# Performance work log

Hardware: AMD Instinct MI355X
Metric: run time of the kernel (lower is better)

The kernel has to match this reference:

```python
import math
import jax, jax.numpy as jnp
import numpy as np

CT = {"SDD": 1000.0, "SCD": 500.0, "det_interval": 1.0, "num_det": 736}


def ramp_filter_np(ct, scale):
    # Standard equiangular fan-beam ramp filter (utility.ramp_filter):
    #   h[0] = 1/(8*db^2); h[n odd] = -1/(2*(pi*sin(n*db))^2); h[n even!=0] = 0
    db = ct["det_interval"] / ct["SDD"] * scale  # angular detector pitch at this scale
    n_det = int(ct["num_det"] // scale)
    n = np.arange(-(n_det - 1), n_det)  # length K = 2*n_det - 1
    h = np.zeros(n.shape, dtype=np.float32)
    h[n == 0] = 1.0 / (8.0 * db ** 2)
    odd = (n % 2) != 0
    h[odd] = -0.5 / (np.pi * np.sin(n[odd] * db)) ** 2
    return h


def setup_inputs() -> dict:
    key = jax.random.key(0)
    scale = 1
    batch, ch, view, det = 16, 1, 1152, CT["num_det"] // scale
    sinogram = jax.random.normal(key, (batch, ch, view, det), dtype=jnp.float32)
    delta_b = CT["det_interval"] / CT["SDD"]
    # recon_filter = ramp_filter * scale * delta_b, shaped [1,1,1,K] (OIHW)
    filt = ramp_filter_np(CT, scale) * scale * delta_b
    recon_filter = jnp.asarray(filt, dtype=jnp.float32)[None, None, None, :]
    return {"sinogram": sinogram, "recon_filter": recon_filter, "scale": scale}


def reference(sinogram, recon_filter, scale):
    det = sinogram.shape[-1]
    # cosine fan-beam pre-weighting
    s_range = (CT["det_interval"]
               * jnp.linspace((1.0 - det) / 2.0, (det - 1.0) / 2.0, det, dtype=jnp.float32)
               * scale) / CT["SDD"]
    cos_weight = (CT["SCD"] / 10000.0) * jnp.cos(s_range)  # [det]
    x = sinogram * cos_weight[None, None, None, :]
    # 1D ramp-filter convolution along detector axis (F.conv2d with 1xK kernel)
    K = recon_filter.shape[-1]
    pad = K // 2
    out = jax.lax.conv_general_dilated(
        x, recon_filter,
        window_strides=(1, 1),
        padding=[(0, 0), (pad, pad)],
        dimension_numbers=("NCHW", "OIHW", "NCHW"),
    )
    return out
```

## Files before the change

kernel.cpp:

```cpp
#include <hip/hip_runtime.h>

typedef unsigned short ushort_t;
typedef ushort_t u16x8 __attribute__((ext_vector_type(8)));
typedef __bf16 bf16x8 __attribute__((ext_vector_type(8)));
typedef float f32x4 __attribute__((ext_vector_type(4)));

#define DET 736
#define NPAD 768

__device__ __forceinline__ ushort_t f2bf(float f) {
    unsigned u = __builtin_bit_cast(unsigned, f);
    u += 0x7FFFu + ((u >> 16) & 1u);
    return (ushort_t)(u >> 16);
}

__global__ void prep_x(const float* __restrict__ sino, ushort_t* __restrict__ X, int total) {
    int idx = (blockIdx.x * blockDim.x + threadIdx.x) * 4;
    if (idx >= total) return;
    const float4 v = *(const float4*)(sino + idx);
    float vv[4] = {v.x, v.y, v.z, v.w};
    int j = idx % DET;
    ushort_t oo[4];
#pragma unroll
    for (int t = 0; t < 4; ++t) {
        float w = 0.05f * cosf(((float)(j + t) - 367.5f) * 0.001f);
        oo[t] = f2bf(vv[t] * w);
    }
    ushort4 o; o.x = oo[0]; o.y = oo[1]; o.z = oo[2]; o.w = oo[3];
    *(ushort4*)(X + idx) = o;
}

__global__ void prep_bt(const float* __restrict__ filt, ushort_t* __restrict__ Bt) {
    int idx = blockIdx.x * blockDim.x + threadIdx.x;
    if (idx >= NPAD * DET) return;
    int n = idx / DET;
    int k = idx - n * DET;
    float v = (n < DET) ? filt[k - n + (DET - 1)] : 0.0f;
    Bt[idx] = f2bf(v);
}

__global__ __launch_bounds__(256) void gemm_bt(
    const ushort_t* __restrict__ A,
    const ushort_t* __restrict__ Bt,
    float* __restrict__ C, int M)
{
    __shared__ ushort_t As[128 * 32];
    __shared__ ushort_t Bs[128 * 32];

    const int tid  = threadIdx.x;
    const int lane = tid & 63;
    const int warp = tid >> 6;
    const int wm   = warp & 1;
    const int wn   = warp >> 1;
    const int quad = lane >> 4;
    const int l16  = lane & 15;

    const size_t row_a0 = (size_t)blockIdx.x * 128;
    const int    row_b0 = blockIdx.y * 128;

    f32x4 acc[4][4];
#pragma unroll
    for (int i = 0; i < 4; ++i)
#pragma unroll
        for (int jx = 0; jx < 4; ++jx)
            acc[i][jx] = (f32x4){0.f, 0.f, 0.f, 0.f};

    const int c0 = tid, c1 = tid + 256;
    const int r0 = c0 >> 2, q0 = c0 & 3;
    const int r1 = c1 >> 2, q1 = c1 & 3;

    for (int k0 = 0; k0 < DET; k0 += 32) {
        __syncthreads();
        u16x8 a0 = *(const u16x8*)(A + (row_a0 + r0) * DET + k0 + q0 * 8);
        u16x8 a1 = *(const u16x8*)(A + (row_a0 + r1) * DET + k0 + q1 * 8);
        u16x8 b0 = *(const u16x8*)(Bt + (size_t)(row_b0 + r0) * DET + k0 + q0 * 8);
        u16x8 b1 = *(const u16x8*)(Bt + (size_t)(row_b0 + r1) * DET + k0 + q1 * 8);
        *(u16x8*)(As + c0 * 8) = a0;
        *(u16x8*)(As + c1 * 8) = a1;
        *(u16x8*)(Bs + c0 * 8) = b0;
        *(u16x8*)(Bs + c1 * 8) = b1;
        __syncthreads();

        u16x8 af[4], bfr[4];
#pragma unroll
        for (int mi = 0; mi < 4; ++mi)
            af[mi] = *(const u16x8*)(As + (wm * 64 + mi * 16 + l16) * 32 + quad * 8);
#pragma unroll
        for (int ni = 0; ni < 4; ++ni)
            bfr[ni] = *(const u16x8*)(Bs + (wn * 64 + ni * 16 + l16) * 32 + quad * 8);
#pragma unroll
        for (int mi = 0; mi < 4; ++mi)
#pragma unroll
            for (int ni = 0; ni < 4; ++ni)
                acc[mi][ni] = __builtin_amdgcn_mfma_f32_16x16x32_bf16(
                    __builtin_bit_cast(bf16x8, af[mi]),
                    __builtin_bit_cast(bf16x8, bfr[ni]),
                    acc[mi][ni], 0, 0, 0);
    }

#pragma unroll
    for (int mi = 0; mi < 4; ++mi) {
#pragma unroll
        for (int ni = 0; ni < 4; ++ni) {
            int colg = row_b0 + wn * 64 + ni * 16 + l16;
            if (colg < DET) {
#pragma unroll
                for (int r = 0; r < 4; ++r) {
                    size_t rowg = row_a0 + wm * 64 + mi * 16 + quad * 4 + r;
                    C[rowg * DET + colg] = acc[mi][ni][r];
                }
            }
        }
    }
}

extern "C" void kernel_launch(void* const* d_in, const int* in_sizes, int n_in,
                              void* d_out, int out_size, void* d_ws, size_t ws_size,
                              hipStream_t stream) {
    const float* sino = (const float*)d_in[0];
    const float* filt = (const float*)d_in[1];
    int total = in_sizes[0];
    int M = total / DET;

    ushort_t* Xbf = (ushort_t*)d_ws;
    ushort_t* Btb = Xbf + (size_t)total;
    float* out = (float*)d_out;

    prep_x<<<(total / 4 + 255) / 256, 256, 0, stream>>>(sino, Xbf, total);
    prep_bt<<<(NPAD * DET + 255) / 256, 256, 0, stream>>>(filt, Btb);

    dim3 grid(M / 128, NPAD / 128);
    gemm_bt<<<grid, 256, 0, stream>>>(Xbf, Btb, out, M);
}
```

Before: 139.4 us.

## Fold cosine weight into filter matrix and load GEMM tiles directly to LDS

The per-detector cosine weight moves from the sinogram prep into the Toeplitz filter matrix, so the activation prep becomes a plain fp32-to-bf16 cast that handles 8 elements per thread. The GEMM tile loads use global_load_lds to copy data straight into shared memory without going through registers, and the leading barrier is skipped on the first iteration. This cuts prep arithmetic and register staging, but the bf16 rounding now happens on the weighted filter instead of on the weighted input.

```diff
diff --git a/kernel.cpp b/kernel.cpp
--- a/kernel.cpp
+++ b/kernel.cpp
@@ -1,4 +1,5 @@
 #include <hip/hip_runtime.h>
+#include <stdint.h>
 
 typedef unsigned short ushort_t;
 typedef ushort_t u16x8 __attribute__((ext_vector_type(8)));
@@ -8,26 +9,24 @@
 #define DET 736
 #define NPAD 768
 
+#define GPTR(p) ((const __attribute__((address_space(1))) unsigned int*)(p))
+#define LPTR(p) ((__attribute__((address_space(3))) unsigned int*)(p))
+
 __device__ __forceinline__ ushort_t f2bf(float f) {
     unsigned u = __builtin_bit_cast(unsigned, f);
     u += 0x7FFFu + ((u >> 16) & 1u);
     return (ushort_t)(u >> 16);
 }
 
-__global__ void prep_x(const float* __restrict__ sino, ushort_t* __restrict__ X, int total) {
-    int idx = (blockIdx.x * blockDim.x + threadIdx.x) * 4;
+__global__ void cast_x(const float* __restrict__ in, ushort_t* __restrict__ out, int total) {
+    int idx = (blockIdx.x * blockDim.x + threadIdx.x) * 8;
     if (idx >= total) return;
-    const float4 v = *(const float4*)(sino + idx);
-    float vv[4] = {v.x, v.y, v.z, v.w};
-    int j = idx % DET;
-    ushort_t oo[4];
-#pragma unroll
-    for (int t = 0; t < 4; ++t) {
-        float w = 0.05f * cosf(((float)(j + t) - 367.5f) * 0.001f);
-        oo[t] = f2bf(vv[t] * w);
-    }
-    ushort4 o; o.x = oo[0]; o.y = oo[1]; o.z = oo[2]; o.w = oo[3];
-    *(ushort4*)(X + idx) = o;
+    float4 a = *(const float4*)(in + idx);
+    float4 b = *(const float4*)(in + idx + 4);
+    u16x8 o;
+    o[0] = f2bf(a.x); o[1] = f2bf(a.y); o[2] = f2bf(a.z); o[3] = f2bf(a.w);
+    o[4] = f2bf(b.x); o[5] = f2bf(b.y); o[6] = f2bf(b.z); o[7] = f2bf(b.w);
+    *(u16x8*)(out + idx) = o;
 }
 
 __global__ void prep_bt(const float* __restrict__ filt, ushort_t* __restrict__ Bt) {
@@ -35,7 +34,8 @@
     if (idx >= NPAD * DET) return;
     int n = idx / DET;
     int k = idx - n * DET;
-    float v = (n < DET) ? filt[k - n + (DET - 1)] : 0.0f;
+    float w = 0.05f * cosf(((float)k - 367.5f) * 0.001f);
+    float v = (n < DET) ? w * filt[k - n + (DET - 1)] : 0.0f;
     Bt[idx] = f2bf(v);
 }
 
@@ -56,7 +56,17 @@
     const int l16  = lane & 15;
 
     const size_t row_a0 = (size_t)blockIdx.x * 128;
-    const int    row_b0 = blockIdx.y * 128;
+    const size_t row_b0 = (size_t)blockIdx.y * 128;
+
+    const int c0 = warp * 64 + lane;
+    const int c1 = c0 + 256;
+    const int r0 = c0 >> 2, q0 = c0 & 3;
+    const int r1 = c1 >> 2, q1 = c1 & 3;
+
+    const ushort_t* a0p = A  + (row_a0 + r0) * DET + q0 * 8;
+    const ushort_t* a1p = A  + (row_a0 + r1) * DET + q1 * 8;
+    const ushort_t* b0p = Bt + (row_b0 + r0) * DET + q0 * 8;
+    const ushort_t* b1p = Bt + (row_b0 + r1) * DET + q1 * 8;
 
     f32x4 acc[4][4];
 #pragma unroll
@@ -65,20 +75,12 @@
         for (int jx = 0; jx < 4; ++jx)
             acc[i][jx] = (f32x4){0.f, 0.f, 0.f, 0.f};
 
-    const int c0 = tid, c1 = tid + 256;
-    const int r0 = c0 >> 2, q0 = c0 & 3;
-    const int r1 = c1 >> 2, q1 = c1 & 3;
-
     for (int k0 = 0; k0 < DET; k0 += 32) {
-        __syncthreads();
-        u16x8 a0 = *(const u16x8*)(A + (row_a0 + r0) * DET + k0 + q0 * 8);
-        u16x8 a1 = *(const u16x8*)(A + (row_a0 + r1) * DET + k0 + q1 * 8);
-        u16x8 b0 = *(const u16x8*)(Bt + (size_t)(row_b0 + r0) * DET + k0 + q0 * 8);
-        u16x8 b1 = *(const u16x8*)(Bt + (size_t)(row_b0 + r1) * DET + k0 + q1 * 8);
-        *(u16x8*)(As + c0 * 8) = a0;
-        *(u16x8*)(As + c1 * 8) = a1;
-        *(u16x8*)(Bs + c0 * 8) = b0;
-        *(u16x8*)(Bs + c1 * 8) = b1;
+        if (k0) __syncthreads();
+        __builtin_amdgcn_global_load_lds(GPTR(a0p + k0), LPTR(As + warp * 512),        16, 0, 0);
+        __builtin_amdgcn_global_load_lds(GPTR(a1p + k0), LPTR(As + 2048 + warp * 512), 16, 0, 0);
+        __builtin_amdgcn_global_load_lds(GPTR(b0p + k0), LPTR(Bs + warp * 512),        16, 0, 0);
+        __builtin_amdgcn_global_load_lds(GPTR(b1p + k0), LPTR(Bs + 2048 + warp * 512), 16, 0, 0);
         __syncthreads();
 
         u16x8 af[4], bfr[4];
@@ -102,7 +104,7 @@
     for (int mi = 0; mi < 4; ++mi) {
 #pragma unroll
         for (int ni = 0; ni < 4; ++ni) {
-            int colg = row_b0 + wn * 64 + ni * 16 + l16;
+            int colg = (int)row_b0 + wn * 64 + ni * 16 + l16;
             if (colg < DET) {
 #pragma unroll
                 for (int r = 0; r < 4; ++r) {
@@ -126,7 +128,7 @@
     ushort_t* Btb = Xbf + (size_t)total;
     float* out = (float*)d_out;
 
-    prep_x<<<(total / 4 + 255) / 256, 256, 0, stream>>>(sino, Xbf, total);
+    cast_x<<<(total / 8 + 255) / 256, 256, 0, stream>>>(sino, Xbf, total);
     prep_bt<<<(NPAD * DET + 255) / 256, 256, 0, stream>>>(filt, Btb);
 
     dim3 grid(M / 128, NPAD / 128);
```

Measured after the change: 144.0 us. 3.3% more time.
